# Kernel optimization log

Measured on AMD Instinct MI355X. Metric: run time of the kernel, lower is better.

The kernel has to match this reference:

```python
import jax, jax.numpy as jnp
import numpy as np
from jax import lax

N_SERIES = 1024   # embedding rows
B = 1024          # batch (= rows of Y)
T = 512           # n_time
INPUT = 28        # input_size
OUTPUT = 28       # output_size
N_T = 2           # temporal exogenous channels
N_S = 4           # static features
M = 7             # seasonality[0]


def setup_inputs() -> dict:
    key = jax.random.key(0)
    k1, k2, k3, k4, k5 = jax.random.split(key, 5)
    S = jax.random.normal(k1, (B, N_S), jnp.float32)
    # Y must be strictly positive (division + log in normalize)
    Y = jax.random.uniform(k2, (B, T), jnp.float32, 0.5, 1.5)
    X = jax.random.normal(k3, (B, N_T, T), jnp.float32)
    idxs = jax.random.randint(k4, (B,), 0, N_SERIES)
    sample_mask = jnp.ones((B, T), jnp.float32)
    # embedding table, init near 0.5 like the torch module
    embeds_weight = 0.5 + 0.05 * jax.random.normal(k5, (N_SERIES, 1 + 1 + M), jnp.float32)
    return dict(S=S, Y=Y, X=X, idxs=idxs, sample_mask=sample_mask,
                embeds_weight=embeds_weight)


def _levels_seasons(Y, embeds):
    """Single-seasonality (len(seasonality)==1) ES recurrence via lax.scan."""
    lev_sms = jax.nn.sigmoid(embeds[:, 0])      # [B]
    seas_sms = jax.nn.sigmoid(embeds[:, 1])     # [B]
    init_seas = jnp.exp(embeds[:, 2:2 + M])     # [B, M]
    s0 = init_seas[:, 0]                        # [B]
    lev0 = Y[:, 0] / s0                         # levels[0] = Y0 / seas_prod
    # seasonalities1 list = [s0..s_{M-1}, s0]; step t uses index t, so the
    # rolling buffer of the next M seasonal values starts as [s1..s_{M-1}, s0]
    buf0 = jnp.concatenate([init_seas[:, 1:], s0[:, None]], axis=1)  # [B, M]

    def step(carry, y_t):
        lev, buf = carry
        seas_t = buf[:, 0]
        newlev = lev_sms * (y_t / seas_t) + (1.0 - lev_sms) * lev
        newseas = seas_sms * (y_t / newlev) + (1.0 - seas_sms) * seas_t
        buf = jnp.concatenate([buf[:, 1:], newseas[:, None]], axis=1)
        return (newlev, buf), (newlev, newseas)

    (_, _), (levs, seass) = lax.scan(step, (lev0, buf0), Y[:, 1:].T)  # [T-1, B]
    levels = jnp.concatenate([lev0[:, None], levs.T], axis=1)         # [B, T]
    init_list = jnp.concatenate([init_seas, s0[:, None]], axis=1)     # [B, M+1]
    seasonalities = jnp.concatenate([init_list, seass.T], axis=1)     # [B, T+M]
    return levels, seasonalities


def _forward_core(S, Y, X, idxs, sample_mask, embeds_weight):
    embeds = embeds_weight[idxs]                    # embedding lookup [B, 9]
    levels, seasonalities = _levels_seasons(Y, embeds)

    W = T - INPUT - OUTPUT + 1                      # n_windows
    starts = jnp.arange(W)
    idx_in = starts[:, None] + jnp.arange(INPUT)    # [W, INPUT]

    Yw = Y[:, idx_in]                               # [B, W, INPUT]
    lev_end = levels[:, starts + INPUT - 1]         # [B, W] level at window end
    seas_in = seasonalities[:, idx_in]              # [B, W, INPUT]
    insample = jnp.log(Yw / (lev_end[:, :, None] * seas_in))  # [B, W, INPUT]

    # temporal exogenous: X[:, :, start:end+OUTPUT].reshape(B, -1)
    idx_x = starts[:, None] + jnp.arange(INPUT + OUTPUT)       # [W, I+O]
    Xw = X[:, :, idx_x]                              # [B, N_T, W, I+O]
    Xw = jnp.transpose(Xw, (0, 2, 1, 3)).reshape(Y.shape[0], W, N_T * (INPUT + OUTPUT))
    insample = jnp.concatenate([insample, Xw], axis=2)

    # static features
    Sw = jnp.broadcast_to(S[:, None, :], (Y.shape[0], W, N_S))
    insample = jnp.concatenate([insample, Sw], axis=2)          # [B, W, C]
    windows_y_insample = jnp.transpose(insample, (1, 0, 2))     # [W, B, C]

    # outsample (eval mode: raw Y, not normalized)
    idx_out = starts[:, None] + INPUT + jnp.arange(OUTPUT)      # [W, OUTPUT]
    windows_y_outsample = jnp.transpose(Y[:, idx_out], (1, 0, 2))  # [W, B, O]

    # sample_mask unfold(size=OUTPUT, step=1), keep last W windows
    n_unf = T - OUTPUT + 1
    starts_m = jnp.arange(n_unf)[-W:]
    idx_m = starts_m[:, None] + jnp.arange(OUTPUT)
    mask_w = jnp.transpose(sample_mask[:, idx_m], (1, 0, 2))    # [W, B, O]

    return windows_y_insample, windows_y_outsample, levels, seasonalities, mask_w


def reference(S, Y, X, idxs, sample_mask, embeds_weight):
    return _forward_core(S, Y, X, idxs, sample_mask, embeds_weight)
```

## Files before the change

### kernel.cpp

```cpp
#include <hip/hip_runtime.h>

#define BB   1024
#define TT   512
#define NIN  28
#define NOUT 28
#define NS   4
#define MM   7
#define WW   457
#define SLEN 519
#define EMB  9

#define OUT1_SZ (WW * BB * 144)
#define OUT2_SZ (WW * BB * 28)
#define OUT3_SZ (BB * TT)
#define OUT4_SZ (BB * SLEN)

#define CH   32
#define NCH  (TT / CH)

typedef float f4 __attribute__((ext_vector_type(4)));

__device__ __forceinline__ f4 ld4u(const float* p) {
    f4 v;
    __builtin_memcpy(&v, p, sizeof(f4));
    return v;
}

__global__ __launch_bounds__(64) void es_scan(const float* __restrict__ Y,
        const int* __restrict__ idxs, const float* __restrict__ EW,
        float* __restrict__ levels, float* __restrict__ seas) {
    __shared__ float yl[64][CH + 1];
    __shared__ float se[64][CH + 1];
    const int tid = threadIdx.x;
    const int b0  = blockIdx.x << 6;
    const int b   = b0 + tid;

    const float* e = EW + idxs[b] * EMB;
    const float lev_sms  = 1.0f / (1.0f + __expf(-e[0]));
    const float seas_sms = 1.0f / (1.0f + __expf(-e[1]));
    const float a_l = 1.0f - lev_sms;
    const float a_s = 1.0f - seas_sms;

    float buf[MM];
    const float is0 = __expf(e[2]);
    {
        float* srow = seas + b * SLEN;
        srow[0] = is0;
#pragma unroll
        for (int k = 1; k < MM; ++k) {
            float v = __expf(e[2 + k]);
            srow[k] = v;
            buf[k - 1] = v;
        }
        buf[MM - 1] = is0;
    }

    f4 pf[8];
#pragma unroll
    for (int k = 0; k < 8; ++k) {
        int flat = (k << 6) + tid;
        int r = flat >> 3, q = flat & 7;
        pf[k] = *reinterpret_cast<const f4*>(Y + (b0 + r) * TT + (q << 2));
    }

    float lev = 0.0f;

#define ES_STEP(TTI)                                                        \
    {                                                                       \
        float y  = yreg[TTI];                                               \
        float st = buf[0];                                                  \
        lev = lev_sms * __fdividef(y, st) + a_l * lev;                      \
        float ns = seas_sms * __fdividef(y, lev) + a_s * st;                \
        buf[0] = buf[1]; buf[1] = buf[2]; buf[2] = buf[3];                  \
        buf[3] = buf[4]; buf[4] = buf[5]; buf[5] = buf[6];                  \
        buf[6] = ns;                                                        \
        yl[tid][TTI] = lev;                                                 \
        se[tid][TTI] = ns;                                                  \
    }

    for (int c = 0; c < NCH; ++c) {
        __syncthreads();
#pragma unroll
        for (int k = 0; k < 8; ++k) {
            int flat = (k << 6) + tid;
            int r = flat >> 3, q = flat & 7;
            float* dst = &yl[r][q << 2];
            dst[0] = pf[k].x; dst[1] = pf[k].y; dst[2] = pf[k].z; dst[3] = pf[k].w;
        }
        __syncthreads();
        if (c < NCH - 1) {
#pragma unroll
            for (int k = 0; k < 8; ++k) {
                int flat = (k << 6) + tid;
                int r = flat >> 3, q = flat & 7;
                pf[k] = *reinterpret_cast<const f4*>(
                    Y + (b0 + r) * TT + (c + 1) * CH + (q << 2));
            }
        }

        float yreg[CH];
#pragma unroll
        for (int tt = 0; tt < CH; ++tt) yreg[tt] = yl[tid][tt];

        if (c == 0) {
            lev = __fdividef(yreg[0], is0);
            yl[tid][0] = lev;
            se[tid][0] = is0;
#pragma unroll
            for (int tt = 1; tt < CH; ++tt) ES_STEP(tt)
        } else {
#pragma unroll
            for (int tt = 0; tt < CH; ++tt) ES_STEP(tt)
        }
        __syncthreads();

#pragma unroll
        for (int k = 0; k < CH; ++k) {
            int flat = (k << 6) + tid;
            int r    = flat >> 5;
            int col  = flat & 31;
            levels[(b0 + r) * TT   + c * CH + col]      = yl[r][col];
            seas  [(b0 + r) * SLEN + MM + c * CH + col] = se[r][col];
        }
    }
#undef ES_STEP
}

#define NA (WW * BB * 28)
#define NB (WW * BB * 8)
#define NC (WW * BB * 7)
#define NTOT (NA + NB + NC)

__global__ __launch_bounds__(256) void main_stream(const float* __restrict__ S,
        const float* __restrict__ Y, const float* __restrict__ X,
        const float* __restrict__ mask, const float* __restrict__ levels,
        const float* __restrict__ seas, f4* __restrict__ out1,
        f4* __restrict__ out2, f4* __restrict__ out5) {
    int i = blockIdx.x * blockDim.x + threadIdx.x;
    const int stride = gridDim.x * blockDim.x;
    for (; i < NTOT; i += stride) {
        if (i < NA) {
            int wb = i / 28;
            int j  = i - wb * 28;
            int b  = wb & (BB - 1);
            int w  = wb >> 10;
            f4 v;
            if (j < 13) {
                v = ld4u(X + (b * 2) * TT + w + ((j + 1) << 2));
            } else if (j < 27) {
                v = ld4u(X + (b * 2 + 1) * TT + w + ((j - 13) << 2));
            } else {
                v = *reinterpret_cast<const f4*>(S + b * NS);
            }
            __builtin_nontemporal_store(v, &out1[wb * 36 + 8 + j]);
        } else if (i < NA + NB) {
            int t  = i - NA;
            int wb = t >> 3;
            int j  = t & 7;
            int b  = wb & (BB - 1);
            int w  = wb >> 10;
            f4 v;
            if (j < 7) {
                int base = w + (j << 2);
                float le = levels[b * TT + w + NIN - 1];
                f4 yv = ld4u(Y    + b * TT   + base);
                f4 sv = ld4u(seas + b * SLEN + base);
                v.x = __logf(__fdividef(yv.x, le * sv.x));
                v.y = __logf(__fdividef(yv.y, le * sv.y));
                v.z = __logf(__fdividef(yv.z, le * sv.z));
                v.w = __logf(__fdividef(yv.w, le * sv.w));
            } else {
                v = ld4u(X + (b * 2) * TT + w);
            }
            __builtin_nontemporal_store(v, &out1[wb * 36 + j]);
        } else {
            int t  = i - (NA + NB);
            int wb = t / 7;
            int j  = t - wb * 7;
            int b  = wb & (BB - 1);
            int w  = wb >> 10;
            int base = w + NIN + (j << 2);
            f4 vy = ld4u(Y    + b * TT + base);
            f4 vm = ld4u(mask + b * TT + base);
            __builtin_nontemporal_store(vy, &out2[wb * 7 + j]);
            __builtin_nontemporal_store(vm, &out5[wb * 7 + j]);
        }
    }
}

extern "C" void kernel_launch(void* const* d_in, const int* in_sizes, int n_in,
                              void* d_out, int out_size, void* d_ws, size_t ws_size,
                              hipStream_t stream) {
    const float* S    = (const float*)d_in[0];
    const float* Y    = (const float*)d_in[1];
    const float* X    = (const float*)d_in[2];
    const int*   idxs = (const int*)d_in[3];
    const float* mask = (const float*)d_in[4];
    const float* EW   = (const float*)d_in[5];

    float* out  = (float*)d_out;
    float* out1 = out;
    float* out2 = out1 + OUT1_SZ;
    float* out3 = out2 + OUT2_SZ;
    float* out4 = out3 + OUT3_SZ;
    float* out5 = out4 + OUT4_SZ;

    es_scan<<<16, 64, 0, stream>>>(Y, idxs, EW, out3, out4);
    main_stream<<<2048, 256, 0, stream>>>(S, Y, X, mask, out3, out4,
                                          (f4*)out1, (f4*)out2, (f4*)out5);
}
```

Measured before the change: 133.4 us.

## Partition main stream kernel by batch groups with contiguous per-block chunks

Splits the batch into 8 groups of 128 rows. Each block now handles one group and walks a contiguous chunk of its work, instead of a grid-stride loop across the whole flattened space. The aim is to keep the X/Y/seas input rows a block reads inside a small working set, so neighbouring windows of the same rows hit in cache. The cost is output writes that are now strided across windows (1024-row stride per window), which may make stores less coalesced.

```diff
diff --git a/kernel.cpp b/kernel.cpp
--- a/kernel.cpp
+++ b/kernel.cpp
@@ -126,24 +126,32 @@
 #undef ES_STEP
 }
 
-#define NA (WW * BB * 28)
-#define NB (WW * BB * 8)
-#define NC (WW * BB * 7)
-#define NTOT (NA + NB + NC)
+#define BGB   128
+#define WBG   (WW * BGB)
+#define NA    (WBG * 28)
+#define NB    (WBG * 8)
+#define NC    (WBG * 7)
+#define NTOTG (NA + NB + NC)
+#define BLKPG 256
+#define CHUNK ((NTOTG + BLKPG - 1) / BLKPG)
 
 __global__ __launch_bounds__(256) void main_stream(const float* __restrict__ S,
         const float* __restrict__ Y, const float* __restrict__ X,
         const float* __restrict__ mask, const float* __restrict__ levels,
         const float* __restrict__ seas, f4* __restrict__ out1,
         f4* __restrict__ out2, f4* __restrict__ out5) {
-    int i = blockIdx.x * blockDim.x + threadIdx.x;
-    const int stride = gridDim.x * blockDim.x;
-    for (; i < NTOT; i += stride) {
+    const int bg   = blockIdx.x & 7;
+    const int blk  = blockIdx.x >> 3;
+    const int bbase = bg << 7;
+    const int start = blk * CHUNK;
+    const int end   = min(start + CHUNK, NTOTG);
+
+    for (int i = start + (int)threadIdx.x; i < end; i += 256) {
         if (i < NA) {
             int wb = i / 28;
             int j  = i - wb * 28;
-            int b  = wb & (BB - 1);
-            int w  = wb >> 10;
+            int b  = bbase + (wb & (BGB - 1));
+            int w  = wb >> 7;
             f4 v;
             if (j < 13) {
                 v = ld4u(X + (b * 2) * TT + w + ((j + 1) << 2));
@@ -152,13 +160,13 @@
             } else {
                 v = *reinterpret_cast<const f4*>(S + b * NS);
             }
-            __builtin_nontemporal_store(v, &out1[wb * 36 + 8 + j]);
+            __builtin_nontemporal_store(v, &out1[((w << 10) + b) * 36 + 8 + j]);
         } else if (i < NA + NB) {
             int t  = i - NA;
             int wb = t >> 3;
             int j  = t & 7;
-            int b  = wb & (BB - 1);
-            int w  = wb >> 10;
+            int b  = bbase + (wb & (BGB - 1));
+            int w  = wb >> 7;
             f4 v;
             if (j < 7) {
                 int base = w + (j << 2);
@@ -172,18 +180,19 @@
             } else {
                 v = ld4u(X + (b * 2) * TT + w);
             }
-            __builtin_nontemporal_store(v, &out1[wb * 36 + j]);
+            __builtin_nontemporal_store(v, &out1[((w << 10) + b) * 36 + j]);
         } else {
             int t  = i - (NA + NB);
             int wb = t / 7;
             int j  = t - wb * 7;
-            int b  = wb & (BB - 1);
-            int w  = wb >> 10;
+            int b  = bbase + (wb & (BGB - 1));
+            int w  = wb >> 7;
             int base = w + NIN + (j << 2);
             f4 vy = ld4u(Y    + b * TT + base);
             f4 vm = ld4u(mask + b * TT + base);
-            __builtin_nontemporal_store(vy, &out2[wb * 7 + j]);
-            __builtin_nontemporal_store(vm, &out5[wb * 7 + j]);
+            int o = ((w << 10) + b) * 7 + j;
+            __builtin_nontemporal_store(vy, &out2[o]);
+            __builtin_nontemporal_store(vm, &out5[o]);
         }
     }
 }
@@ -206,6 +215,6 @@
     float* out5 = out4 + OUT4_SZ;
 
     es_scan<<<16, 64, 0, stream>>>(Y, idxs, EW, out3, out4);
-    main_stream<<<2048, 256, 0, stream>>>(S, Y, X, mask, out3, out4,
-                                          (f4*)out1, (f4*)out2, (f4*)out5);
-}
+    main_stream<<<8 * BLKPG, 256, 0, stream>>>(S, Y, X, mask, out3, out4,
+                                               (f4*)out1, (f4*)out2, (f4*)out5);
+}
```

After: 164.8 us. 23.6% more time.
